# Optimization experiments

Measured on AMD Instinct MI355X. Metric: run time of the kernel, lower is better.

## Reference

```python
import jax, jax.numpy as jnp
import numpy as np

N, IN_DIM, OUT_DIM, H = 8192, 128, 128, 2
HD = OUT_DIM // H
NEG_SLOPE = 0.2


def setup_inputs() -> dict:
    key = jax.random.key(0)
    k1, k2, k3, k4, k5 = jax.random.split(key, 5)
    x = jax.random.normal(k1, (N, IN_DIM), dtype=jnp.float32)
    adj = jax.random.randint(k2, (N, N), 0, 2).astype(jnp.float32)
    W = jax.random.normal(k3, (IN_DIM, OUT_DIM), dtype=jnp.float32) / np.sqrt(IN_DIM)
    a_src = jax.random.normal(k4, (H, HD), dtype=jnp.float32) * 0.01
    a_dst = jax.random.normal(k5, (H, HD), dtype=jnp.float32) * 0.01
    return {"x": x, "adj": adj, "W": W, "a_src": a_src, "a_dst": a_dst}


def reference(x, adj, W, a_src, a_dst):
    # h: (N, H, HD)
    h = (x @ W).reshape(N, H, HD)
    # per-node additive score halves: (N, H)
    e_src = jnp.einsum('nhd,hd->nh', h, a_src)
    e_dst = jnp.einsum('nhd,hd->nh', h, a_dst)
    # attn logits: (N_i, N_j, H); torch code adds e_src[i] + e_dst[j]
    logits = jax.nn.leaky_relu(e_src[:, None, :] + e_dst[None, :, :], NEG_SLOPE)
    logits = jnp.where(adj[:, :, None] > 0, logits, -jnp.inf)
    # softmax over neighbor axis j (dim=1), matching F.softmax(attn, dim=1)
    attn = jax.nn.softmax(logits, axis=1)
    # dropout omitted (eval mode)
    out = jnp.einsum('ijh,jhd->ihd', attn, h).reshape(N, OUT_DIM)
    return out
```

## Files before the change

### kernel.cpp

```cpp
#include <hip/hip_runtime.h>
#include <hip/hip_bf16.h>

#define N 8192
#define IND 128
#define OUTD 128
#define JC 8
#define JLEN 1024
#define SUBC 8
#define SUBJ 128
#define TSUB 4
#define NW64 (N / 64)

typedef float f32x4 __attribute__((ext_vector_type(4)));
typedef short s16x8 __attribute__((ext_vector_type(8)));
typedef _Float16 f16;
typedef _Float16 f16x2 __attribute__((ext_vector_type(2)));
typedef _Float16 f16x4 __attribute__((ext_vector_type(4)));
typedef long long ll2 __attribute__((ext_vector_type(2)));
typedef unsigned int u32x4 __attribute__((ext_vector_type(4)));

static __device__ inline unsigned short f2bf(float f) {
    union { float f; unsigned u; } v; v.f = f;
    unsigned u = v.u + 0x7fffu + ((v.u >> 16) & 1u);
    return (unsigned short)(u >> 16);
}
static __device__ inline float bf2f(unsigned short b) {
    union { unsigned u; float f; } v; v.u = ((unsigned)b) << 16;
    return v.f;
}
static __device__ __forceinline__ unsigned pkbf(float a, float b) {
    __hip_bfloat162 t = __float22bfloat162_rn(make_float2(a, b));
    unsigned u;
    __builtin_memcpy(&u, &t, 4);
    return u;
}
static __device__ __forceinline__ void async16(const void* g, void* l) {
    __builtin_amdgcn_global_load_lds(
        (const __attribute__((address_space(1))) unsigned int*)g,
        (__attribute__((address_space(3))) unsigned int*)l, 16, 0, 0);
}

__global__ __launch_bounds__(256) void k0_pack(const float* __restrict__ adj,
                                               unsigned long long* __restrict__ bits) {
    const int row = blockIdx.x;
    const int wave = threadIdx.x >> 6, lane = threadIdx.x & 63;
    const float* src = adj + (size_t)row * N + wave * 2048;
    unsigned long long acc = 0;
#pragma unroll
    for (int t = 0; t < 32; ++t) {
        float v = src[t * 64 + lane];
        unsigned long long b = __ballot(v != 0.0f);
        if (lane == t) acc = b;
    }
    if (lane < 32)
        bits[(size_t)row * NW64 + wave * 32 + lane] = acc;
}

__global__ __launch_bounds__(256) void k1_xw(const float* __restrict__ x,
                                             const float* __restrict__ W,
                                             unsigned short* __restrict__ hT) {
    __shared__ unsigned short Wl[128 * 130];
    const int tid = threadIdx.x;
    {
        int k = tid >> 1, n0 = (tid & 1) * 64;
        const float4* src = (const float4*)(W + k * 128 + n0);
#pragma unroll
        for (int v = 0; v < 16; ++v) {
            float4 f = src[v];
            int base = k * 130 + n0 + v * 4;
            Wl[base + 0] = f2bf(f.x);
            Wl[base + 1] = f2bf(f.y);
            Wl[base + 2] = f2bf(f.z);
            Wl[base + 3] = f2bf(f.w);
        }
    }
    __syncthreads();
    const int wave = tid >> 6, lane = tid & 63;
    const int m = lane & 15, quad = lane >> 4;
    const int ibase = blockIdx.x * 64 + wave * 16;
    const int irow = ibase + m;

    f32x4 acc[8];
#pragma unroll
    for (int t = 0; t < 8; ++t) acc[t] = (f32x4){0.f, 0.f, 0.f, 0.f};

#pragma unroll
    for (int ks = 0; ks < 4; ++ks) {
        const int k0 = ks * 32 + quad * 8;
        const float4* xp = (const float4*)(x + (size_t)irow * 128 + k0);
        float4 xa = xp[0], xb = xp[1];
        s16x8 afrag;
        afrag[0] = (short)f2bf(xa.x); afrag[1] = (short)f2bf(xa.y);
        afrag[2] = (short)f2bf(xa.z); afrag[3] = (short)f2bf(xa.w);
        afrag[4] = (short)f2bf(xb.x); afrag[5] = (short)f2bf(xb.y);
        afrag[6] = (short)f2bf(xb.z); afrag[7] = (short)f2bf(xb.w);
#pragma unroll
        for (int nt = 0; nt < 8; ++nt) {
            const int n = nt * 16 + m;
            s16x8 bfrag;
#pragma unroll
            for (int j = 0; j < 8; ++j)
                bfrag[j] = (short)Wl[(k0 + j) * 130 + n];
            acc[nt] = __builtin_amdgcn_mfma_f32_16x16x32_bf16(afrag, bfrag, acc[nt], 0, 0, 0);
        }
    }
#pragma unroll
    for (int nt = 0; nt < 8; ++nt) {
        const int c = nt * 16 + m;
        const int i0 = ibase + quad * 4;
        ushort4 pk;
        pk.x = f2bf(acc[nt][0]); pk.y = f2bf(acc[nt][1]);
        pk.z = f2bf(acc[nt][2]); pk.w = f2bf(acc[nt][3]);
        *(ushort4*)(hT + (size_t)c * N + i0) = pk;
    }
}

__global__ __launch_bounds__(256) void k2_e(const unsigned short* __restrict__ hT,
                                            const float* __restrict__ a_src,
                                            const float* __restrict__ a_dst,
                                            float* __restrict__ As, float* __restrict__ Cs,
                                            uint2* __restrict__ BDh) {
    const int i = blockIdx.x * 256 + threadIdx.x;
    float es0 = 0.f, ed0 = 0.f, es1 = 0.f, ed1 = 0.f;
#pragma unroll 8
    for (int c = 0; c < 128; ++c) {
        float v = bf2f(hT[(size_t)c * N + i]);
        float as = a_src[c], ad = a_dst[c];
        if (c < 64) { es0 += v * as; ed0 += v * ad; }
        else        { es1 += v * as; ed1 += v * ad; }
    }
    As[i]     = __expf(es0);
    As[N + i] = __expf(es1);
    Cs[i]     = __expf(0.2f * es0);
    Cs[N + i] = __expf(0.2f * es1);
    uint2 bd;
    bd.x = pkbf(__expf(ed0), __expf(0.2f * ed0));
    bd.y = pkbf(__expf(ed1), __expf(0.2f * ed1));
    BDh[i] = bd;
}

__global__ __launch_bounds__(256, 4) void k3_main(const unsigned long long* __restrict__ bits,
                                                  const unsigned short* __restrict__ hTg,
                                                  const float* __restrict__ As,
                                                  const float* __restrict__ Cs,
                                                  const uint2* __restrict__ BDh,
                                                  f16* __restrict__ Up,
                                                  float* __restrict__ Lp) {
    __shared__ float4 smem4[2112];
    unsigned short* hTl = (unsigned short*)smem4;
    uint2* bdl = (uint2*)((char*)smem4 + 32768);
    const int tid = threadIdx.x;
    const int wave = tid >> 6, lane = tid & 63;
    const int m = lane & 15, quad = lane >> 4;
    const int ibase = blockIdx.x * 64 + wave * 16;
    const int irow = ibase + m;
    const int jc = blockIdx.y;
    const int j0 = jc * JLEN;

    const float A0 = As[irow], C0 = Cs[irow];
    const float A1 = As[N + irow], C1 = Cs[N + irow];

    f32x4 acc[2][4];
#pragma unroll
    for (int h = 0; h < 2; ++h)
#pragma unroll
        for (int nt = 0; nt < 4; ++nt) acc[h][nt] = (f32x4){0.f, 0.f, 0.f, 0.f};
    f32x4 accS[2];
    accS[0] = (f32x4){0.f, 0.f, 0.f, 0.f};
    accS[1] = (f32x4){0.f, 0.f, 0.f, 0.f};

    s16x8 ones;
#pragma unroll
    for (int t = 0; t < 8; ++t) ones[t] = (short)0x3F80;

    const int crow = lane >> 4;
    const int gd = lane & 15;

#pragma unroll 1
    for (int sc = 0; sc < SUBC; ++sc) {
        const int jb = j0 + sc * SUBJ;
        if (sc) __syncthreads();
        ll2 mk = *(const ll2*)(bits + (size_t)irow * NW64 + (jb >> 6));
        if (wave == 0)
            async16(BDh + jb + lane * 2, bdl);
#pragma unroll
        for (int rr = 0; rr < 8; ++rr) {
            const int rg = wave * 8 + rr;
            const int c = rg * 4 + crow;
            const int gs = gd ^ (c & 7);
            async16(hTg + (size_t)c * N + jb + gs * 8, hTl + rg * 512);
        }
        __syncthreads();

#pragma unroll
        for (int t = 0; t < TSUB; ++t) {
            u32x4 bq[4];
            const u32x4* bp = (const u32x4*)(bdl + (t * 32 + quad * 8));
#pragma unroll
            for (int z = 0; z < 4; ++z) bq[z] = bp[z];
            s16x8 h0[4], h1[4];
            const int gr = t * 4 + quad;
#pragma unroll
            for (int nt = 0; nt < 4; ++nt) {
                const int c0 = nt * 16 + m;
                const int go = (gr ^ (c0 & 7)) * 8;
                h0[nt] = *(const s16x8*)(hTl + c0 * 128 + go);
                h1[nt] = *(const s16x8*)(hTl + (c0 + 64) * 128 + go);
            }
            const unsigned long long mw =
                (t < 2) ? (unsigned long long)mk[0] : (unsigned long long)mk[1];
            const unsigned mbyte = (unsigned)(mw >> ((t & 1) * 32 + quad * 8)) & 0xffu;

            float pv0[8], pv1[8];
#pragma unroll
            for (int jj = 0; jj < 8; ++jj) {
                const unsigned p0u = bq[jj >> 1][(jj & 1) * 2];
                const unsigned p1u = bq[jj >> 1][(jj & 1) * 2 + 1];
                float B0 = __uint_as_float(p0u << 16);
                float D0 = __uint_as_float(p0u & 0xffff0000u);
                float B1 = __uint_as_float(p1u << 16);
                float D1 = __uint_as_float(p1u & 0xffff0000u);
                float w0 = fmaxf(A0 * B0, C0 * D0);
                float w1 = fmaxf(A1 * B1, C1 * D1);
                bool on = (mbyte >> jj) & 1u;
                pv0[jj] = on ? w0 : 0.0f;
                pv1[jj] = on ? w1 : 0.0f;
            }
            unsigned pu0[4], pu1[4];
#pragma unroll
            for (int q = 0; q < 4; ++q) {
                pu0[q] = pkbf(pv0[q * 2], pv0[q * 2 + 1]);
                pu1[q] = pkbf(pv1[q * 2], pv1[q * 2 + 1]);
            }
            s16x8 p0, p1;
            __builtin_memcpy(&p0, pu0, 16);
            __builtin_memcpy(&p1, pu1, 16);

#pragma unroll
            for (int nt = 0; nt < 4; ++nt) {
                acc[0][nt] = __builtin_amdgcn_mfma_f32_16x16x32_bf16(p0, h0[nt], acc[0][nt], 0, 0, 0);
                acc[1][nt] = __builtin_amdgcn_mfma_f32_16x16x32_bf16(p1, h1[nt], acc[1][nt], 0, 0, 0);
            }
            accS[0] = __builtin_amdgcn_mfma_f32_16x16x32_bf16(p0, ones, accS[0], 0, 0, 0);
            accS[1] = __builtin_amdgcn_mfma_f32_16x16x32_bf16(p1, ones, accS[1], 0, 0, 0);
        }
    }

    __syncthreads();
    float* smf = (float*)smem4 + wave * (16 * 129);
#pragma unroll
    for (int h = 0; h < 2; ++h)
#pragma unroll
        for (int nt = 0; nt < 4; ++nt) {
            const int c = h * 64 + nt * 16 + m;
#pragma unroll
            for (int r = 0; r < 4; ++r)
                smf[(quad * 4 + r) * 129 + c] = acc[h][nt][r];
        }
    f16* Ub = Up + (size_t)jc * N * 128;
#pragma unroll
    for (int r16 = 0; r16 < 16; ++r16) {
        float v0 = smf[r16 * 129 + lane * 2];
        float v1 = smf[r16 * 129 + lane * 2 + 1];
        f16x2 pk; pk[0] = (f16)v0; pk[1] = (f16)v1;
        *(f16x2*)(Ub + (size_t)(ibase + r16) * 128 + lane * 2) = pk;
    }
    if (m == 0) {
#pragma unroll
        for (int h = 0; h < 2; ++h)
#pragma unroll
            for (int r = 0; r < 4; ++r)
                Lp[((size_t)jc * 2 + h) * N + ibase + quad * 4 + r] = accS[h][r];
    }
}

__global__ __launch_bounds__(256) void k4_reduce(const f16* __restrict__ Up,
                                                 const float* __restrict__ Lp,
                                                 float* __restrict__ out) {
    const int base = (blockIdx.x * 256 + threadIdx.x) * 4;
    const int i = base >> 7, c = base & 127, h = c >> 6;
    float su0 = 0.f, su1 = 0.f, su2 = 0.f, su3 = 0.f, sl = 0.f;
#pragma unroll
    for (int jcc = 0; jcc < JC; ++jcc) {
        f16x4 u = *(const f16x4*)(Up + (size_t)jcc * N * 128 + base);
        su0 += (float)u[0]; su1 += (float)u[1];
        su2 += (float)u[2]; su3 += (float)u[3];
        sl += Lp[((size_t)jcc * 2 + h) * N + i];
    }
    float inv = 1.0f / sl;
    float4 o; o.x = su0 * inv; o.y = su1 * inv; o.z = su2 * inv; o.w = su3 * inv;
    *(float4*)(out + base) = o;
}

extern "C" void kernel_launch(void* const* d_in, const int* in_sizes, int n_in,
                              void* d_out, int out_size, void* d_ws, size_t ws_size,
                              hipStream_t stream) {
    const float* x     = (const float*)d_in[0];
    const float* adj   = (const float*)d_in[1];
    const float* W     = (const float*)d_in[2];
    const float* a_src = (const float*)d_in[3];
    const float* a_dst = (const float*)d_in[4];
    float* out = (float*)d_out;
    char* ws = (char*)d_ws;

    size_t off = 0;
    unsigned short* hT = (unsigned short*)(ws + off); off += (size_t)128 * N * 2;
    float* As = (float*)(ws + off); off += (size_t)2 * N * 4;
    float* Cs = (float*)(ws + off); off += (size_t)2 * N * 4;
    uint2* BDh = (uint2*)(ws + off); off += (size_t)N * 8;
    unsigned long long* bits = (unsigned long long*)(ws + off); off += (size_t)N * NW64 * 8;
    f16* Up = (f16*)(ws + off); off += (size_t)JC * N * 128 * 2;
    float* Lp = (float*)(ws + off); off += (size_t)JC * 2 * N * 4;

    k0_pack<<<N, 256, 0, stream>>>(adj, bits);
    k1_xw<<<N / 64, 256, 0, stream>>>(x, W, hT);
    k2_e<<<N / 256, 256, 0, stream>>>(hT, a_src, a_dst, As, Cs, BDh);
    dim3 g3(N / 64, JC);
    k3_main<<<g3, 256, 0, stream>>>(bits, hT, As, Cs, BDh, Up, Lp);
    k4_reduce<<<(N * 128) / (256 * 4), 256, 0, stream>>>(Up, Lp, out);
}
```

Measured before the change: 436.2 us.

## Process two row tiles per wave, permute j order, and vectorize adjacency packing

The main attention kernel now has each wave handle 32 rows (two 16-row groups), so every hT fragment read from LDS feeds twice as many MFMAs. The j-chunk count goes to 16 with shorter chunks to keep the grid large. The j axis is permuted in hT and BD so the mask bits a quad needs come from one 32-bit word. The pack kernel reads adj as float4 and emits 32-bit words with a matching bit order. This adds register pressure (occupancy hint lowered to 3) and doubles the partial-sum buffers that the reduce kernel must read.

```diff
diff --git a/kernel.cpp b/kernel.cpp
--- a/kernel.cpp
+++ b/kernel.cpp
@@ -4,19 +4,16 @@
 #define N 8192
 #define IND 128
 #define OUTD 128
-#define JC 8
-#define JLEN 1024
-#define SUBC 8
-#define SUBJ 128
+#define JC 16
+#define JLEN 512
+#define SUBC 4
 #define TSUB 4
-#define NW64 (N / 64)
 
 typedef float f32x4 __attribute__((ext_vector_type(4)));
 typedef short s16x8 __attribute__((ext_vector_type(8)));
 typedef _Float16 f16;
 typedef _Float16 f16x2 __attribute__((ext_vector_type(2)));
 typedef _Float16 f16x4 __attribute__((ext_vector_type(4)));
-typedef long long ll2 __attribute__((ext_vector_type(2)));
 typedef unsigned int u32x4 __attribute__((ext_vector_type(4)));
 
 static __device__ inline unsigned short f2bf(float f) {
@@ -39,26 +36,40 @@
         (const __attribute__((address_space(1))) unsigned int*)g,
         (__attribute__((address_space(3))) unsigned int*)l, 16, 0, 0);
 }
+static __device__ __forceinline__ unsigned qsel(u32x4 v, int quad) {
+    unsigned a = (quad & 1) ? v[1] : v[0];
+    unsigned b = (quad & 1) ? v[3] : v[2];
+    return (quad & 2) ? b : a;
+}
 
 __global__ __launch_bounds__(256) void k0_pack(const float* __restrict__ adj,
-                                               unsigned long long* __restrict__ bits) {
+                                               unsigned int* __restrict__ bits32) {
     const int row = blockIdx.x;
     const int wave = threadIdx.x >> 6, lane = threadIdx.x & 63;
-    const float* src = adj + (size_t)row * N + wave * 2048;
-    unsigned long long acc = 0;
-#pragma unroll
-    for (int t = 0; t < 32; ++t) {
-        float v = src[t * 64 + lane];
-        unsigned long long b = __ballot(v != 0.0f);
-        if (lane == t) acc = b;
-    }
-    if (lane < 32)
-        bits[(size_t)row * NW64 + wave * 32 + lane] = acc;
+    const float4* src = (const float4*)(adj + (size_t)row * N + wave * 2048);
+    unsigned acc = 0;
+#pragma unroll
+    for (int it = 0; it < 8; ++it) {
+        float4 v = src[it * 64 + lane];
+        unsigned long long b0 = __ballot(v.x != 0.0f);
+        unsigned long long b1 = __ballot(v.y != 0.0f);
+        unsigned long long b2 = __ballot(v.z != 0.0f);
+        unsigned long long b3 = __ballot(v.w != 0.0f);
+        unsigned w[8];
+        w[0] = (unsigned)b0; w[1] = (unsigned)b1;
+        w[2] = (unsigned)b2; w[3] = (unsigned)b3;
+        w[4] = (unsigned)(b0 >> 32); w[5] = (unsigned)(b1 >> 32);
+        w[6] = (unsigned)(b2 >> 32); w[7] = (unsigned)(b3 >> 32);
+#pragma unroll
+        for (int z = 0; z < 8; ++z)
+            acc = (lane == it * 8 + z) ? w[z] : acc;
+    }
+    bits32[(size_t)row * 256 + wave * 64 + lane] = acc;
 }
 
 __global__ __launch_bounds__(256) void k1_xw(const float* __restrict__ x,
                                              const float* __restrict__ W,
-                                             unsigned short* __restrict__ hT) {
+                                             unsigned short* __restrict__ hTp) {
     __shared__ unsigned short Wl[128 * 130];
     const int tid = threadIdx.x;
     {
@@ -77,8 +88,8 @@
     __syncthreads();
     const int wave = tid >> 6, lane = tid & 63;
     const int m = lane & 15, quad = lane >> 4;
-    const int ibase = blockIdx.x * 64 + wave * 16;
-    const int irow = ibase + m;
+    const int T = blockIdx.x * 64 + wave * 16;
+    const int arow = T + 4 * (m & 3) + (m >> 2);
 
     f32x4 acc[8];
 #pragma unroll
@@ -87,7 +98,7 @@
 #pragma unroll
     for (int ks = 0; ks < 4; ++ks) {
         const int k0 = ks * 32 + quad * 8;
-        const float4* xp = (const float4*)(x + (size_t)irow * 128 + k0);
+        const float4* xp = (const float4*)(x + (size_t)arow * 128 + k0);
         float4 xa = xp[0], xb = xp[1];
         s16x8 afrag;
         afrag[0] = (short)f2bf(xa.x); afrag[1] = (short)f2bf(xa.y);
@@ -104,46 +115,47 @@
             acc[nt] = __builtin_amdgcn_mfma_f32_16x16x32_bf16(afrag, bfrag, acc[nt], 0, 0, 0);
         }
     }
+    const int sbase = blockIdx.x * 64 + (wave & 2) * 16 + quad * 8 + (wave & 1) * 4;
 #pragma unroll
     for (int nt = 0; nt < 8; ++nt) {
         const int c = nt * 16 + m;
-        const int i0 = ibase + quad * 4;
         ushort4 pk;
         pk.x = f2bf(acc[nt][0]); pk.y = f2bf(acc[nt][1]);
         pk.z = f2bf(acc[nt][2]); pk.w = f2bf(acc[nt][3]);
-        *(ushort4*)(hT + (size_t)c * N + i0) = pk;
-    }
-}
-
-__global__ __launch_bounds__(256) void k2_e(const unsigned short* __restrict__ hT,
+        *(ushort4*)(hTp + (size_t)c * N + sbase) = pk;
+    }
+}
+
+__global__ __launch_bounds__(256) void k2_e(const unsigned short* __restrict__ hTp,
                                             const float* __restrict__ a_src,
                                             const float* __restrict__ a_dst,
                                             float* __restrict__ As, float* __restrict__ Cs,
-                                            uint2* __restrict__ BDh) {
-    const int i = blockIdx.x * 256 + threadIdx.x;
+                                            uint2* __restrict__ BDp) {
+    const int s = blockIdx.x * 256 + threadIdx.x;
+    const int n = (s & ~31) | ((s & 7) << 2) | ((s >> 3) & 3);
     float es0 = 0.f, ed0 = 0.f, es1 = 0.f, ed1 = 0.f;
 #pragma unroll 8
     for (int c = 0; c < 128; ++c) {
-        float v = bf2f(hT[(size_t)c * N + i]);
+        float v = bf2f(hTp[(size_t)c * N + s]);
         float as = a_src[c], ad = a_dst[c];
         if (c < 64) { es0 += v * as; ed0 += v * ad; }
         else        { es1 += v * as; ed1 += v * ad; }
     }
-    As[i]     = __expf(es0);
-    As[N + i] = __expf(es1);
-    Cs[i]     = __expf(0.2f * es0);
-    Cs[N + i] = __expf(0.2f * es1);
+    As[n]     = __expf(es0);
+    As[N + n] = __expf(es1);
+    Cs[n]     = __expf(0.2f * es0);
+    Cs[N + n] = __expf(0.2f * es1);
     uint2 bd;
     bd.x = pkbf(__expf(ed0), __expf(0.2f * ed0));
     bd.y = pkbf(__expf(ed1), __expf(0.2f * ed1));
-    BDh[i] = bd;
-}
-
-__global__ __launch_bounds__(256, 4) void k3_main(const unsigned long long* __restrict__ bits,
-                                                  const unsigned short* __restrict__ hTg,
+    BDp[s] = bd;
+}
+
+__global__ __launch_bounds__(256, 3) void k3_main(const unsigned int* __restrict__ bits32,
+                                                  const unsigned short* __restrict__ hTp,
                                                   const float* __restrict__ As,
                                                   const float* __restrict__ Cs,
-                                                  const uint2* __restrict__ BDh,
+                                                  const uint2* __restrict__ BDp,
                                                   f16* __restrict__ Up,
                                                   float* __restrict__ Lp) {
     __shared__ float4 smem4[2112];
@@ -152,22 +164,23 @@
     const int tid = threadIdx.x;
     const int wave = tid >> 6, lane = tid & 63;
     const int m = lane & 15, quad = lane >> 4;
-    const int ibase = blockIdx.x * 64 + wave * 16;
-    const int irow = ibase + m;
+    const int ibase = blockIdx.x * 128 + wave * 32;
+    const int ra = ibase + m, rb = ibase + 16 + m;
     const int jc = blockIdx.y;
     const int j0 = jc * JLEN;
 
-    const float A0 = As[irow], C0 = Cs[irow];
-    const float A1 = As[N + irow], C1 = Cs[N + irow];
-
-    f32x4 acc[2][4];
-#pragma unroll
-    for (int h = 0; h < 2; ++h)
-#pragma unroll
-        for (int nt = 0; nt < 4; ++nt) acc[h][nt] = (f32x4){0.f, 0.f, 0.f, 0.f};
-    f32x4 accS[2];
-    accS[0] = (f32x4){0.f, 0.f, 0.f, 0.f};
-    accS[1] = (f32x4){0.f, 0.f, 0.f, 0.f};
+    const float A0a = As[ra], C0a = Cs[ra], A1a = As[N + ra], C1a = Cs[N + ra];
+    const float A0b = As[rb], C0b = Cs[rb], A1b = As[N + rb], C1b = Cs[N + rb];
+
+    f32x4 acc[2][2][4];
+#pragma unroll
+    for (int g = 0; g < 2; ++g)
+#pragma unroll
+        for (int h = 0; h < 2; ++h)
+#pragma unroll
+            for (int nt = 0; nt < 4; ++nt) acc[g][h][nt] = (f32x4){0.f, 0.f, 0.f, 0.f};
+    f32x4 accS[2][2];
+    accS[0][0] = accS[0][1] = accS[1][0] = accS[1][1] = (f32x4){0.f, 0.f, 0.f, 0.f};
 
     s16x8 ones;
 #pragma unroll
@@ -178,19 +191,23 @@
 
 #pragma unroll 1
     for (int sc = 0; sc < SUBC; ++sc) {
-        const int jb = j0 + sc * SUBJ;
+        const int jb = j0 + sc * 128;
         if (sc) __syncthreads();
-        ll2 mk = *(const ll2*)(bits + (size_t)irow * NW64 + (jb >> 6));
+        u32x4 mka = *(const u32x4*)(bits32 + (size_t)ra * 256 + (jb >> 5));
+        u32x4 mkb = *(const u32x4*)(bits32 + (size_t)rb * 256 + (jb >> 5));
         if (wave == 0)
-            async16(BDh + jb + lane * 2, bdl);
+            async16(BDp + jb + lane * 2, bdl);
 #pragma unroll
         for (int rr = 0; rr < 8; ++rr) {
             const int rg = wave * 8 + rr;
             const int c = rg * 4 + crow;
             const int gs = gd ^ (c & 7);
-            async16(hTg + (size_t)c * N + jb + gs * 8, hTl + rg * 512);
+            async16(hTp + (size_t)c * N + jb + gs * 8, hTl + rg * 512);
         }
         __syncthreads();
+
+        const unsigned wa = qsel(mka, quad);
+        const unsigned wb = qsel(mkb, quad);
 
 #pragma unroll
         for (int t = 0; t < TSUB; ++t) {
@@ -198,79 +215,85 @@
             const u32x4* bp = (const u32x4*)(bdl + (t * 32 + quad * 8));
 #pragma unroll
             for (int z = 0; z < 4; ++z) bq[z] = bp[z];
-            s16x8 h0[4], h1[4];
-            const int gr = t * 4 + quad;
+            const unsigned mba = (wa >> (t * 8)) & 0xffu;
+            const unsigned mbb = (wb >> (t * 8)) & 0xffu;
+
+            float pa0[8], pa1[8], pb0[8], pb1[8];
+#pragma unroll
+            for (int jj = 0; jj < 8; ++jj) {
+                const unsigned u0 = bq[jj >> 1][(jj & 1) * 2];
+                const unsigned u1 = bq[jj >> 1][(jj & 1) * 2 + 1];
+                float B0 = __uint_as_float(u0 << 16);
+                float D0 = __uint_as_float(u0 & 0xffff0000u);
+                float B1 = __uint_as_float(u1 << 16);
+                float D1 = __uint_as_float(u1 & 0xffff0000u);
+                bool oa = (mba >> jj) & 1u;
+                bool ob = (mbb >> jj) & 1u;
+                pa0[jj] = oa ? fmaxf(A0a * B0, C0a * D0) : 0.0f;
+                pa1[jj] = oa ? fmaxf(A1a * B1, C1a * D1) : 0.0f;
+                pb0[jj] = ob ? fmaxf(A0b * B0, C0b * D0) : 0.0f;
+                pb1[jj] = ob ? fmaxf(A1b * B1, C1b * D1) : 0.0f;
+            }
+            unsigned qa0[4], qa1[4], qb0[4], qb1[4];
+#pragma unroll
+            for (int q = 0; q < 4; ++q) {
+                qa0[q] = pkbf(pa0[q * 2], pa0[q * 2 + 1]);
+                qa1[q] = pkbf(pa1[q * 2], pa1[q * 2 + 1]);
+                qb0[q] = pkbf(pb0[q * 2], pb0[q * 2 + 1]);
+                qb1[q] = pkbf(pb1[q * 2], pb1[q * 2 + 1]);
+            }
+            s16x8 p0a, p1a, p0b, p1b;
+            __builtin_memcpy(&p0a, qa0, 16);
+            __builtin_memcpy(&p1a, qa1, 16);
+            __builtin_memcpy(&p0b, qb0, 16);
+            __builtin_memcpy(&p1b, qb1, 16);
+
 #pragma unroll
             for (int nt = 0; nt < 4; ++nt) {
                 const int c0 = nt * 16 + m;
-                const int go = (gr ^ (c0 & 7)) * 8;
-                h0[nt] = *(const s16x8*)(hTl + c0 * 128 + go);
-                h1[nt] = *(const s16x8*)(hTl + (c0 + 64) * 128 + go);
+                const int go = ((t * 4 + quad) ^ (c0 & 7)) * 8;
+                s16x8 h0 = *(const s16x8*)(hTl + c0 * 128 + go);
+                s16x8 h1 = *(const s16x8*)(hTl + (c0 + 64) * 128 + go);
+                acc[0][0][nt] = __builtin_amdgcn_mfma_f32_16x16x32_bf16(p0a, h0, acc[0][0][nt], 0, 0, 0);
+                acc[1][0][nt] = __builtin_amdgcn_mfma_f32_16x16x32_bf16(p0b, h0, acc[1][0][nt], 0, 0, 0);
+                acc[0][1][nt] = __builtin_amdgcn_mfma_f32_16x16x32_bf16(p1a, h1, acc[0][1][nt], 0, 0, 0);
+                acc[1][1][nt] = __builtin_amdgcn_mfma_f32_16x16x32_bf16(p1b, h1, acc[1][1][nt], 0, 0, 0);
             }
-            const unsigned long long mw =
-                (t < 2) ? (unsigned long long)mk[0] : (unsigned long long)mk[1];
-            const unsigned mbyte = (unsigned)(mw >> ((t & 1) * 32 + quad * 8)) & 0xffu;
-
-            float pv0[8], pv1[8];
-#pragma unroll
-            for (int jj = 0; jj < 8; ++jj) {
-                const unsigned p0u = bq[jj >> 1][(jj & 1) * 2];
-                const unsigned p1u = bq[jj >> 1][(jj & 1) * 2 + 1];
-                float B0 = __uint_as_float(p0u << 16);
-                float D0 = __uint_as_float(p0u & 0xffff0000u);
-                float B1 = __uint_as_float(p1u << 16);
-                float D1 = __uint_as_float(p1u & 0xffff0000u);
-                float w0 = fmaxf(A0 * B0, C0 * D0);
-                float w1 = fmaxf(A1 * B1, C1 * D1);
-                bool on = (mbyte >> jj) & 1u;
-                pv0[jj] = on ? w0 : 0.0f;
-                pv1[jj] = on ? w1 : 0.0f;
-            }
-            unsigned pu0[4], pu1[4];
-#pragma unroll
-            for (int q = 0; q < 4; ++q) {
-                pu0[q] = pkbf(pv0[q * 2], pv0[q * 2 + 1]);
-                pu1[q] = pkbf(pv1[q * 2], pv1[q * 2 + 1]);
-            }
-            s16x8 p0, p1;
-            __builtin_memcpy(&p0, pu0, 16);
-            __builtin_memcpy(&p1, pu1, 16);
-
-#pragma unroll
-            for (int nt = 0; nt < 4; ++nt) {
-                acc[0][nt] = __builtin_amdgcn_mfma_f32_16x16x32_bf16(p0, h0[nt], acc[0][nt], 0, 0, 0);
-                acc[1][nt] = __builtin_amdgcn_mfma_f32_16x16x32_bf16(p1, h1[nt], acc[1][nt], 0, 0, 0);
-            }
-            accS[0] = __builtin_amdgcn_mfma_f32_16x16x32_bf16(p0, ones, accS[0], 0, 0, 0);
-            accS[1] = __builtin_amdgcn_mfma_f32_16x16x32_bf16(p1, ones, accS[1], 0, 0, 0);
+            accS[0][0] = __builtin_amdgcn_mfma_f32_16x16x32_bf16(p0a, ones, accS[0][0], 0, 0, 0);
+            accS[0][1] = __builtin_amdgcn_mfma_f32_16x16x32_bf16(p1a, ones, accS[0][1], 0, 0, 0);
+            accS[1][0] = __builtin_amdgcn_mfma_f32_16x16x32_bf16(p0b, ones, accS[1][0], 0, 0, 0);
+            accS[1][1] = __builtin_amdgcn_mfma_f32_16x16x32_bf16(p1b, ones, accS[1][1], 0, 0, 0);
         }
     }
 
     __syncthreads();
     float* smf = (float*)smem4 + wave * (16 * 129);
-#pragma unroll
-    for (int h = 0; h < 2; ++h)
-#pragma unroll
-        for (int nt = 0; nt < 4; ++nt) {
-            const int c = h * 64 + nt * 16 + m;
-#pragma unroll
-            for (int r = 0; r < 4; ++r)
-                smf[(quad * 4 + r) * 129 + c] = acc[h][nt][r];
-        }
     f16* Ub = Up + (size_t)jc * N * 128;
 #pragma unroll
-    for (int r16 = 0; r16 < 16; ++r16) {
-        float v0 = smf[r16 * 129 + lane * 2];
-        float v1 = smf[r16 * 129 + lane * 2 + 1];
-        f16x2 pk; pk[0] = (f16)v0; pk[1] = (f16)v1;
-        *(f16x2*)(Ub + (size_t)(ibase + r16) * 128 + lane * 2) = pk;
-    }
-    if (m == 0) {
+    for (int g = 0; g < 2; ++g) {
 #pragma unroll
         for (int h = 0; h < 2; ++h)
 #pragma unroll
-            for (int r = 0; r < 4; ++r)
-                Lp[((size_t)jc * 2 + h) * N + ibase + quad * 4 + r] = accS[h][r];
+            for (int nt = 0; nt < 4; ++nt) {
+                const int c = h * 64 + nt * 16 + m;
+#pragma unroll
+                for (int r = 0; r < 4; ++r)
+                    smf[(quad * 4 + r) * 129 + c] = acc[g][h][nt][r];
+            }
+#pragma unroll
+        for (int r16 = 0; r16 < 16; ++r16) {
+            float v0 = smf[r16 * 129 + lane * 2];
+            float v1 = smf[r16 * 129 + lane * 2 + 1];
+            f16x2 pk; pk[0] = (f16)v0; pk[1] = (f16)v1;
+            *(f16x2*)(Ub + (size_t)(ibase + g * 16 + r16) * 128 + lane * 2) = pk;
+        }
+        if (m == 0) {
+#pragma unroll
+            for (int h = 0; h < 2; ++h)
+#pragma unroll
+                for (int r = 0; r < 4; ++r)
+                    Lp[((size_t)jc * 2 + h) * N + ibase + g * 16 + quad * 4 + r] = accS[g][h][r];
+        }
     }
 }
 
@@ -304,18 +327,18 @@
     char* ws = (char*)d_ws;
 
     size_t off = 0;
-    unsigned short* hT = (unsigned short*)(ws + off); off += (size_t)128 * N * 2;
+    unsigned short* hTp = (unsigned short*)(ws + off); off += (size_t)128 * N * 2;
     float* As = (float*)(ws + off); off += (size_t)2 * N * 4;
     float* Cs = (float*)(ws + off); off += (size_t)2 * N * 4;
-    uint2* BDh = (uint2*)(ws + off); off += (size_t)N * 8;
-    unsigned long long* bits = (unsigned long long*)(ws + off); off += (size_t)N * NW64 * 8;
+    uint2* BDp = (uint2*)(ws + off); off += (size_t)N * 8;
+    unsigned int* bits32 = (unsigned int*)(ws + off); off += (size_t)N * 256 * 4;
     f16* Up = (f16*)(ws + off); off += (size_t)JC * N * 128 * 2;
     float* Lp = (float*)(ws + off); off += (size_t)JC * 2 * N * 4;
 
-    k0_pack<<<N, 256, 0, stream>>>(adj, bits);
-    k1_xw<<<N / 64, 256, 0, stream>>>(x, W, hT);
-    k2_e<<<N / 256, 256, 0, stream>>>(hT, a_src, a_dst, As, Cs, BDh);
-    dim3 g3(N / 64, JC);
-    k3_main<<<g3, 256, 0, stream>>>(bits, hT, As, Cs, BDh, Up, Lp);
+    k0_pack<<<N, 256, 0, stream>>>(adj, bits32);
+    k1_xw<<<N / 64, 256, 0, stream>>>(x, W, hTp);
+    k2_e<<<N / 256, 256, 0, stream>>>(hTp, a_src, a_dst, As, Cs, BDp);
+    dim3 g3(N / 128, JC);
+    k3_main<<<g3, 256, 0, stream>>>(bits32, hTp, As, Cs, BDp, Up, Lp);
     k4_reduce<<<(N * 128) / (256 * 4), 256, 0, stream>>>(Up, Lp, out);
 }
```

After: 445.8 us. 2.2% more time.

## Halve j-chunk length and LDS tile to double grid and raise occupancy

Applied to the files above, without the earlier changes.

Splits the neighbor axis into 16 chunks of 512 instead of 8 of 1024 and halves each LDS sub-tile to 64 columns. This halves shared memory per block so launch bounds can request 6 blocks per CU, and it doubles the number of blocks to fill more compute units. The epilogue is rewritten to stage one head at a time through a smaller LDS buffer. The cost is twice as many partial U/L outputs to write and reduce, plus more barriers per unit of work.

```diff
diff --git a/kernel.cpp b/kernel.cpp
--- a/kernel.cpp
+++ b/kernel.cpp
@@ -4,19 +4,17 @@
 #define N 8192
 #define IND 128
 #define OUTD 128
-#define JC 8
-#define JLEN 1024
+#define JC 16
+#define JLEN 512
 #define SUBC 8
-#define SUBJ 128
-#define TSUB 4
+#define SUBJ 64
+#define TSUB 2
 #define NW64 (N / 64)
 
 typedef float f32x4 __attribute__((ext_vector_type(4)));
 typedef short s16x8 __attribute__((ext_vector_type(8)));
 typedef _Float16 f16;
-typedef _Float16 f16x2 __attribute__((ext_vector_type(2)));
 typedef _Float16 f16x4 __attribute__((ext_vector_type(4)));
-typedef long long ll2 __attribute__((ext_vector_type(2)));
 typedef unsigned int u32x4 __attribute__((ext_vector_type(4)));
 
 static __device__ inline unsigned short f2bf(float f) {
@@ -139,16 +137,16 @@
     BDh[i] = bd;
 }
 
-__global__ __launch_bounds__(256, 4) void k3_main(const unsigned long long* __restrict__ bits,
+__global__ __launch_bounds__(256, 6) void k3_main(const unsigned long long* __restrict__ bits,
                                                   const unsigned short* __restrict__ hTg,
                                                   const float* __restrict__ As,
                                                   const float* __restrict__ Cs,
                                                   const uint2* __restrict__ BDh,
                                                   f16* __restrict__ Up,
                                                   float* __restrict__ Lp) {
-    __shared__ float4 smem4[2112];
+    __shared__ float4 smem4[1056];
     unsigned short* hTl = (unsigned short*)smem4;
-    uint2* bdl = (uint2*)((char*)smem4 + 32768);
+    uint2* bdl = (uint2*)((char*)smem4 + 16384);
     const int tid = threadIdx.x;
     const int wave = tid >> 6, lane = tid & 63;
     const int m = lane & 15, quad = lane >> 4;
@@ -173,20 +171,20 @@
 #pragma unroll
     for (int t = 0; t < 8; ++t) ones[t] = (short)0x3F80;
 
-    const int crow = lane >> 4;
-    const int gd = lane & 15;
+    const int crow = lane >> 3;
+    const int gd = lane & 7;
 
 #pragma unroll 1
     for (int sc = 0; sc < SUBC; ++sc) {
         const int jb = j0 + sc * SUBJ;
         if (sc) __syncthreads();
-        ll2 mk = *(const ll2*)(bits + (size_t)irow * NW64 + (jb >> 6));
-        if (wave == 0)
+        const unsigned long long mk = bits[(size_t)irow * NW64 + (jb >> 6)];
+        if (wave == 0 && lane < 32)
             async16(BDh + jb + lane * 2, bdl);
 #pragma unroll
-        for (int rr = 0; rr < 8; ++rr) {
-            const int rg = wave * 8 + rr;
-            const int c = rg * 4 + crow;
+        for (int rr = 0; rr < 4; ++rr) {
+            const int rg = wave * 4 + rr;
+            const int c = rg * 8 + crow;
             const int gs = gd ^ (c & 7);
             async16(hTg + (size_t)c * N + jb + gs * 8, hTl + rg * 512);
         }
@@ -199,27 +197,25 @@
 #pragma unroll
             for (int z = 0; z < 4; ++z) bq[z] = bp[z];
             s16x8 h0[4], h1[4];
-            const int gr = t * 4 + quad;
+            const int gq = t * 4 + quad;
 #pragma unroll
             for (int nt = 0; nt < 4; ++nt) {
                 const int c0 = nt * 16 + m;
-                const int go = (gr ^ (c0 & 7)) * 8;
-                h0[nt] = *(const s16x8*)(hTl + c0 * 128 + go);
-                h1[nt] = *(const s16x8*)(hTl + (c0 + 64) * 128 + go);
+                const int go = (gq ^ (c0 & 7)) * 8;
+                h0[nt] = *(const s16x8*)(hTl + c0 * 64 + go);
+                h1[nt] = *(const s16x8*)(hTl + (c0 + 64) * 64 + go);
             }
-            const unsigned long long mw =
-                (t < 2) ? (unsigned long long)mk[0] : (unsigned long long)mk[1];
-            const unsigned mbyte = (unsigned)(mw >> ((t & 1) * 32 + quad * 8)) & 0xffu;
+            const unsigned mbyte = (unsigned)(mk >> (t * 32 + quad * 8)) & 0xffu;
 
             float pv0[8], pv1[8];
 #pragma unroll
             for (int jj = 0; jj < 8; ++jj) {
-                const unsigned p0u = bq[jj >> 1][(jj & 1) * 2];
-                const unsigned p1u = bq[jj >> 1][(jj & 1) * 2 + 1];
-                float B0 = __uint_as_float(p0u << 16);
-                float D0 = __uint_as_float(p0u & 0xffff0000u);
-                float B1 = __uint_as_float(p1u << 16);
-                float D1 = __uint_as_float(p1u & 0xffff0000u);
+                const unsigned u0 = bq[jj >> 1][(jj & 1) * 2];
+                const unsigned u1 = bq[jj >> 1][(jj & 1) * 2 + 1];
+                float B0 = __uint_as_float(u0 << 16);
+                float D0 = __uint_as_float(u0 & 0xffff0000u);
+                float B1 = __uint_as_float(u1 << 16);
+                float D1 = __uint_as_float(u1 & 0xffff0000u);
                 float w0 = fmaxf(A0 * B0, C0 * D0);
                 float w1 = fmaxf(A1 * B1, C1 * D1);
                 bool on = (mbyte >> jj) & 1u;
@@ -247,23 +243,22 @@
     }
 
     __syncthreads();
-    float* smf = (float*)smem4 + wave * (16 * 129);
-#pragma unroll
-    for (int h = 0; h < 2; ++h)
+    float* smf = (float*)smem4 + wave * (16 * 66);
+    f16* Ub = Up + (size_t)jc * N * 128;
+#pragma unroll
+    for (int h = 0; h < 2; ++h) {
 #pragma unroll
         for (int nt = 0; nt < 4; ++nt) {
-            const int c = h * 64 + nt * 16 + m;
+            const int c = nt * 16 + m;
 #pragma unroll
             for (int r = 0; r < 4; ++r)
-                smf[(quad * 4 + r) * 129 + c] = acc[h][nt][r];
-        }
-    f16* Ub = Up + (size_t)jc * N * 128;
-#pragma unroll
-    for (int r16 = 0; r16 < 16; ++r16) {
-        float v0 = smf[r16 * 129 + lane * 2];
-        float v1 = smf[r16 * 129 + lane * 2 + 1];
-        f16x2 pk; pk[0] = (f16)v0; pk[1] = (f16)v1;
-        *(f16x2*)(Ub + (size_t)(ibase + r16) * 128 + lane * 2) = pk;
+                smf[(quad * 4 + r) * 66 + c] = acc[h][nt][r];
+        }
+#pragma unroll
+        for (int r16 = 0; r16 < 16; ++r16) {
+            float v = smf[r16 * 66 + lane];
+            Ub[(size_t)(ibase + r16) * 128 + h * 64 + lane] = (f16)v;
+        }
     }
     if (m == 0) {
 #pragma unroll
```

After: 486.2 us. +11.5%, slower.
